# Performance work log

Measured on AMD Instinct MI355X. Metric: run time of the kernel, lower is better.

Reference implementation:

```python
import jax, jax.numpy as jnp
import numpy as np


def _kernel_features(data, proj, is_query):
    # data: [B,S,H,D], proj: [R,D] -> features [B,S,H,R]  (FAVOR+ positive softmax kernel)
    d = data.shape[-1]
    r = proj.shape[0]
    data_normalizer = 1.0 / jnp.sqrt(jnp.sqrt(jnp.float32(d)))
    ratio = 1.0 / jnp.sqrt(jnp.float32(r))
    data_hat = jnp.einsum('bshd,rd->bshr', data_normalizer * data, proj)
    diag = (jnp.sum(data * data, axis=-1) * 0.5) * (data_normalizer * data_normalizer)
    diag = diag[..., None]  # [B,S,H,1]
    if is_query:
        m = jnp.max(data_hat, axis=-1, keepdims=True)
    else:
        m = jnp.max(data_hat)
    return ratio * (jnp.exp(data_hat - diag - m) + 1e-4)


def reference(query, key, value, Wq, bq, Wk, bk, Wv, bv, Wo, bo, proj):
    proj = jax.lax.stop_gradient(proj)
    # QKV projections: [B,S,Dm] -> [B,S,H,Dh]
    q = jnp.einsum('bsd,dhk->bshk', query, Wq) + bq
    k = jnp.einsum('bsd,dhk->bshk', key, Wk) + bk
    v = jnp.einsum('bsd,dhv->bshv', value, Wv) + bv
    q_hat = _kernel_features(q, proj, True)   # [B,S,H,R]
    k_hat = _kernel_features(k, proj, False)  # [B,S,H,R]
    # kv aggregation: 'aecr,aecd->acrd'
    kv = jnp.einsum('bshr,bshv->bhrv', k_hat, v)          # [B,H,R,Dv]
    out = jnp.einsum('bshr,bhrv->bshv', q_hat, kv)        # [B,S,H,Dv]
    # normalization: k1 = sum_s k_hat ('abcd,abc->acd'), denom = q_hat . k1
    k1 = jnp.sum(k_hat, axis=1)                           # [B,H,R]
    denom = jnp.einsum('bshr,bhr->bsh', q_hat, k1)        # [B,S,H]
    out = out / denom[..., None]
    # output projection: combine heads
    return jnp.einsum('bshv,hvd->bsd', out, Wo) + bo


def setup_inputs() -> dict:
    key0 = jax.random.key(0)
    ks = jax.random.split(key0, 10)
    B, S, Dm, H, Dh, R = 4, 4096, 1024, 16, 64, 256
    scale = 1.0 / np.sqrt(Dm)
    # Gaussian orthogonal random matrix [R, Dh], scaling=0 (chi row norms)
    blk = jax.random.normal(ks[8], (R, Dh))
    qmat, _ = jnp.linalg.qr(blk)  # R >= Dh -> q is [R, Dh]
    mult = jnp.linalg.norm(jax.random.normal(ks[9], (R, Dh)), axis=1)
    proj = mult[:, None] * qmat
    return {
        'query': jax.random.normal(ks[0], (B, S, Dm)),
        'key': jax.random.normal(ks[1], (B, S, Dm)),
        'value': jax.random.normal(ks[2], (B, S, Dm)),
        'Wq': jax.random.normal(ks[3], (Dm, H, Dh)) * scale,
        'bq': jnp.zeros((H, Dh)),
        'Wk': jax.random.normal(ks[4], (Dm, H, Dh)) * scale,
        'bk': jnp.zeros((H, Dh)),
        'Wv': jax.random.normal(ks[5], (Dm, H, Dh)) * scale,
        'bv': jnp.zeros((H, Dh)),
        'Wo': jax.random.normal(ks[6], (H, Dh, Dm)) * scale,
        'bo': jnp.zeros((Dm,)),
        'proj': proj,
    }
```

## Files before the change

### kernel.cpp

```cpp
#include <hip/hip_runtime.h>

typedef unsigned short u16;
typedef unsigned int u32;
typedef __attribute__((ext_vector_type(4))) float f32x4;
typedef __attribute__((ext_vector_type(8))) short bf16x8;

#define B_ 4
#define S_ 4096
#define H_ 16
#define DH_ 64
#define R_ 256
#define DM_ 1024
#define M_ 16384
#define ROWSTR 1024

__device__ __forceinline__ float bf2f(u16 u) {
  union { u32 i; float f; } v; v.i = ((u32)u) << 16; return v.f;
}
__device__ __forceinline__ u16 f2bf(float f) {
  union { float f; u32 i; } v; v.f = f;
  u32 x = v.i;
  return (u16)((x + 0x7FFFu + ((x >> 16) & 1u)) >> 16);
}
__device__ __forceinline__ void lds_load16(const void* g, void* l) {
  __builtin_amdgcn_global_load_lds((__attribute__((address_space(1))) void*)(g),
                                   (__attribute__((address_space(3))) void*)(l), 16, 0, 0);
}
__device__ __forceinline__ int vt_idx(int dv, int s) {
  return dv * 64 + (s ^ (dv & 0x38));
}

__global__ __launch_bounds__(256) void dtype_probe_k(const u16* __restrict__ q,
                                                     int* __restrict__ flag) {
  __shared__ int cnt_s;
  int tid = threadIdx.x;
  if (tid == 0) cnt_s = 0;
  __syncthreads();
  int c = 0;
  for (int i = tid; i < 1024; i += 256) {
    u32 e = ((u32)q[i] >> 7) & 0xFF;
    c += (e >= 134) ? 1 : 0;
  }
  atomicAdd(&cnt_s, c);
  __syncthreads();
  if (tid == 0) flag[0] = (cnt_s > 32) ? 1 : 0;
}

template <int WLO>
__global__ __launch_bounds__(256) void split_k(const void* __restrict__ src,
                                               u16* __restrict__ hi, u16* __restrict__ lo,
                                               const int* __restrict__ flag) {
  const bool f32m = flag[0] != 0;
  size_t i = ((size_t)blockIdx.x * 256 + threadIdx.x) * 8;
  if (f32m) {
    f32x4 a = *(const f32x4*)((const float*)src + i);
    f32x4 b = *(const f32x4*)((const float*)src + i + 4);
    bf16x8 h, l;
    for (int e = 0; e < 4; ++e) {
      u16 ha = f2bf(a[e]); h[e] = (short)ha; l[e] = (short)f2bf(a[e] - bf2f(ha));
      u16 hb = f2bf(b[e]); h[4 + e] = (short)hb; l[4 + e] = (short)f2bf(b[e] - bf2f(hb));
    }
    *(bf16x8*)(hi + i) = h;
    if (WLO) *(bf16x8*)(lo + i) = l;
  } else {
    bf16x8 h = *(const bf16x8*)((const u16*)src + i);
    *(bf16x8*)(hi + i) = h;
    if (WLO) {
      bf16x8 z = {0, 0, 0, 0, 0, 0, 0, 0};
      *(bf16x8*)(lo + i) = z;
    }
  }
}

__global__ __launch_bounds__(256) void transpose4_k(
    const void* __restrict__ s0, const void* __restrict__ s1,
    const void* __restrict__ s2, const void* __restrict__ s3,
    u16* __restrict__ dh0, u16* __restrict__ dl0, u16* __restrict__ dh1, u16* __restrict__ dl1,
    u16* __restrict__ dh2, u16* __restrict__ dl2, u16* __restrict__ dh3, u16* __restrict__ dl3,
    const int* __restrict__ flag) {
  __shared__ float tile[32][33];
  const bool f32m = flag[0] != 0;
  int z = blockIdx.z;
  const void* src = (z == 0) ? s0 : (z == 1) ? s1 : (z == 2) ? s2 : s3;
  u16* dh = (z == 0) ? dh0 : (z == 1) ? dh1 : (z == 2) ? dh2 : dh3;
  u16* dl = (z == 0) ? dl0 : (z == 1) ? dl1 : (z == 2) ? dl2 : dl3;
  int tx = threadIdx.x, ty = threadIdx.y;
  int x0 = blockIdx.x * 32, y0 = blockIdx.y * 32;
  for (int i = ty; i < 32; i += 8) {
    size_t idx = (size_t)(y0 + i) * DM_ + x0 + tx;
    tile[i][tx] = f32m ? ((const float*)src)[idx] : bf2f(((const u16*)src)[idx]);
  }
  __syncthreads();
  for (int i = ty; i < 32; i += 8) {
    float t = tile[tx][i];
    u16 hi = f2bf(t);
    size_t o = (size_t)(x0 + i) * DM_ + y0 + tx;
    dh[o] = hi;
    dl[o] = f2bf(t - bf2f(hi));
  }
}

__global__ __launch_bounds__(256) void projcvt_k(const void* __restrict__ p,
                                                 u16* __restrict__ ph, u16* __restrict__ pl,
                                                 const int* __restrict__ flag) {
  const bool f32m = flag[0] != 0;
  int i = blockIdx.x * 256 + threadIdx.x;
  if (i < R_ * DH_) {
    float t = f32m ? ((const float*)p)[i] : bf2f(((const u16*)p)[i]);
    u16 hi = f2bf(t);
    ph[i] = hi;
    pl[i] = f2bf(t - bf2f(hi));
  }
}

template <int PREC, int OUTMODE>
__global__ __launch_bounds__(256) void gemm_k(
    const u16* __restrict__ Ah, const u16* __restrict__ Al,
    const u16* __restrict__ Bth, const u16* __restrict__ Btl,
    const void* __restrict__ bias, void* __restrict__ C, u16* __restrict__ Clo,
    const int* __restrict__ flag) {
  constexpr int NPL = (PREC == 3) ? 4 : 2;
  __shared__ __attribute__((aligned(16))) u16 pool[2 * NPL * 4096];
  const bool f32m = flag[0] != 0;
  const int K = DM_, N = DM_;
  const int tid = threadIdx.x, wave = tid >> 6, lane = tid & 63;
  const int lr = lane & 15, qd = lane >> 4;
  const int bm = blockIdx.x, bn = blockIdx.y;
  const int m0 = (wave & 1) * 64, n0 = (wave >> 1) * 64;
  const u16* Abh = Ah + (size_t)bm * 128 * K;
  const u16* Bbh = Bth + (size_t)bn * 128 * K;
  const u16* Abl = (PREC == 3) ? Al + (size_t)bm * 128 * K : nullptr;
  const u16* Bbl = (PREC == 3) ? Btl + (size_t)bn * 128 * K : nullptr;
  f32x4 zero = {0.f, 0.f, 0.f, 0.f};
  f32x4 acc[4][4];
  for (int i = 0; i < 4; ++i) for (int j = 0; j < 4; ++j) acc[i][j] = zero;

#define GEMM_STAGE(bf, kk)                                             \
  do {                                                                 \
    u16* Ph_ = pool + (bf) * (NPL * 4096);                             \
    for (int t_ = 0; t_ < 2; ++t_) {                                   \
      int c_ = wave + t_ * 4;                                          \
      int row_ = c_ * 16 + (lane >> 2);                                \
      int kc_ = (lane & 3) * 8;                                        \
      size_t go_ = (size_t)row_ * K + (kk) + kc_;                      \
      lds_load16(Abh + go_, (void*)&Ph_[c_ * 512]);                    \
      lds_load16(Bbh + go_, (void*)&Ph_[4096 + c_ * 512]);             \
      if (PREC == 3) {                                                 \
        lds_load16(Abl + go_, (void*)&Ph_[2 * 4096 + c_ * 512]);       \
        lds_load16(Bbl + go_, (void*)&Ph_[3 * 4096 + c_ * 512]);       \
      }                                                                \
    }                                                                  \
  } while (0)

  GEMM_STAGE(0, 0);
  int cur = 0;
  for (int k0 = 0; k0 < K; k0 += 32) {
    __syncthreads();
    if (k0 + 32 < K) GEMM_STAGE(cur ^ 1, k0 + 32);
    const u16* Ph = pool + cur * (NPL * 4096);
    const u16* Ash = Ph;
    const u16* Bsh = Ph + 4096;
    bf16x8 ah[4], bh[4];
    for (int i = 0; i < 4; ++i) ah[i] = *(const bf16x8*)&Ash[(m0 + i * 16 + lr) * 32 + qd * 8];
    for (int j = 0; j < 4; ++j) bh[j] = *(const bf16x8*)&Bsh[(n0 + j * 16 + lr) * 32 + qd * 8];
    for (int i = 0; i < 4; ++i)
      for (int j = 0; j < 4; ++j)
        acc[i][j] = __builtin_amdgcn_mfma_f32_16x16x32_bf16(ah[i], bh[j], acc[i][j], 0, 0, 0);
    if (PREC == 3) {
      const u16* Asl = Ph + 2 * 4096;
      const u16* Bsl = Ph + 3 * 4096;
      bf16x8 al[4], bl[4];
      for (int i = 0; i < 4; ++i) al[i] = *(const bf16x8*)&Asl[(m0 + i * 16 + lr) * 32 + qd * 8];
      for (int j = 0; j < 4; ++j) bl[j] = *(const bf16x8*)&Bsl[(n0 + j * 16 + lr) * 32 + qd * 8];
      for (int i = 0; i < 4; ++i)
        for (int j = 0; j < 4; ++j) {
          acc[i][j] = __builtin_amdgcn_mfma_f32_16x16x32_bf16(ah[i], bl[j], acc[i][j], 0, 0, 0);
          acc[i][j] = __builtin_amdgcn_mfma_f32_16x16x32_bf16(al[i], bh[j], acc[i][j], 0, 0, 0);
        }
    }
    cur ^= 1;
  }
#undef GEMM_STAGE
  for (int j = 0; j < 4; ++j) {
    int n = bn * 128 + n0 + j * 16 + lr;
    float bv = f32m ? ((const float*)bias)[n] : bf2f(((const u16*)bias)[n]);
    for (int i = 0; i < 4; ++i) {
      int mr = bm * 128 + m0 + i * 16 + qd * 4;
      for (int r2 = 0; r2 < 4; ++r2) {
        float x = acc[i][j][r2] + bv;
        size_t o = (size_t)(mr + r2) * N + n;
        if (OUTMODE == 0) {
          ((u16*)C)[o] = f2bf(x);
        } else if (OUTMODE == 1) {
          u16 hi = f2bf(x);
          ((u16*)C)[o] = hi;
          Clo[o] = f2bf(x - bf2f(hi));
        } else {
          if (f32m) ((float*)C)[o] = x;
          else ((u16*)C)[o] = f2bf(x);
        }
      }
    }
  }
}

__global__ __launch_bounds__(256) void feat_max_k(
    const u16* __restrict__ khi, const u16* __restrict__ klo,
    const u16* __restrict__ ph, const u16* __restrict__ pl, float* __restrict__ pm) {
  __shared__ __attribute__((aligned(16))) u16 kth[64 * 64];
  __shared__ __attribute__((aligned(16))) u16 ktl[64 * 64];
  __shared__ float red[4];
  const int tid = threadIdx.x, wave = tid >> 6, lane = tid & 63;
  const int lr = lane & 15, qd = lane >> 4;
  int bid = blockIdx.x;
  int chunk = bid & 63, bh = bid >> 6;
  int b = bh >> 4, h = bh & 15;
  size_t base = (((size_t)b * S_ + (size_t)chunk * 64) * H_ + h) * DH_;
  for (int t = 0; t < 2; ++t) {
    int cc = wave + t * 4;
    int rr = cc * 8 + (lane >> 3);
    int csw = (((lane & 7) ^ (rr & 7)) << 3);
    size_t go = base + (size_t)rr * ROWSTR + csw;
    lds_load16(khi + go, (void*)&kth[cc * 512]);
    lds_load16(klo + go, (void*)&ktl[cc * 512]);
  }
  __syncthreads();
  const int r0 = wave * 64;
  f32x4 zero = {0.f, 0.f, 0.f, 0.f};
  f32x4 acc[4][4];
  for (int i = 0; i < 4; ++i) for (int j = 0; j < 4; ++j) acc[i][j] = zero;
  __builtin_amdgcn_s_setprio(1);
  for (int ks = 0; ks < 2; ++ks) {
    bf16x8 ah[4], al[4], bh_[4], bl_[4];
    for (int i = 0; i < 4; ++i) {
      int cof = (ks * 32 + qd * 8) ^ ((lr & 7) << 3);
      ah[i] = *(const bf16x8*)&kth[(i * 16 + lr) * 64 + cof];
      al[i] = *(const bf16x8*)&ktl[(i * 16 + lr) * 64 + cof];
    }
    for (int j = 0; j < 4; ++j) {
      size_t o = (size_t)(r0 + j * 16 + lr) * DH_ + ks * 32 + qd * 8;
      bh_[j] = *(const bf16x8*)(ph + o);
      bl_[j] = *(const bf16x8*)(pl + o);
    }
    for (int i = 0; i < 4; ++i)
      for (int j = 0; j < 4; ++j) {
        acc[i][j] = __builtin_amdgcn_mfma_f32_16x16x32_bf16(ah[i], bh_[j], acc[i][j], 0, 0, 0);
        acc[i][j] = __builtin_amdgcn_mfma_f32_16x16x32_bf16(al[i], bh_[j], acc[i][j], 0, 0, 0);
        acc[i][j] = __builtin_amdgcn_mfma_f32_16x16x32_bf16(ah[i], bl_[j], acc[i][j], 0, 0, 0);
      }
  }
  __builtin_amdgcn_s_setprio(0);
  float mx = -3.0e38f;
  for (int i = 0; i < 4; ++i) for (int j = 0; j < 4; ++j) for (int r2 = 0; r2 < 4; ++r2)
    mx = fmaxf(mx, acc[i][j][r2]);
  for (int m2 = 1; m2 < 64; m2 <<= 1) mx = fmaxf(mx, __shfl_xor(mx, m2, 64));
  if (lane == 0) red[wave] = mx;
  __syncthreads();
  if (tid == 0)
    pm[bid] = 0.3535533905932738f * fmaxf(fmaxf(red[0], red[1]), fmaxf(red[2], red[3]));
}

__global__ __launch_bounds__(256) void reduce_max_k(const float* __restrict__ pm,
                                                    float* __restrict__ mout) {
  __shared__ float buf[256];
  int t = threadIdx.x;
  float m = -3.0e38f;
  for (int i = t; i < 4096; i += 256) m = fmaxf(m, pm[i]);
  buf[t] = m;
  __syncthreads();
  if (t < 64) {
    float v = fmaxf(fmaxf(buf[t], buf[t + 64]), fmaxf(buf[t + 128], buf[t + 192]));
    for (int m2 = 1; m2 < 64; m2 <<= 1) v = fmaxf(v, __shfl_xor(v, m2, 64));
    if (t == 0) mout[0] = v;
  }
}

__global__ __launch_bounds__(256) void kv_accum_k(
    const u16* __restrict__ khi, const u16* __restrict__ klo,
    const u16* __restrict__ vv,
    const u16* __restrict__ ph, const u16* __restrict__ pl,
    const float* __restrict__ mptr,
    float* __restrict__ pkv, float* __restrict__ pk1, int ipb) {
  __shared__ __attribute__((aligned(16))) u16 pool[256 * 72];
  __shared__ __attribute__((aligned(16))) u16 vTh[64 * 64];
  __shared__ float dpart[4][64];
  __shared__ float diagl[64];
  u16* kth = pool;
  u16* ktl = pool + 4096;
  u16* khatT = pool;
  const int tid = threadIdx.x, wave = tid >> 6, lane = tid & 63;
  const int lr = lane & 15, qd = lane >> 4;
  int bid = blockIdx.x;
  int bh = bid & 63, c = bid >> 6;
  int b = bh >> 4, h = bh & 15;
  const float mglob = mptr[0];
  const float nrm = 0.3535533905932738f;
  const float ratio = 0.0625f;
  size_t base0 = (((size_t)b * S_ + (size_t)c * ipb * 64) * H_ + h) * DH_;
  f32x4 zero = {0.f, 0.f, 0.f, 0.f};
  f32x4 acc[4][4];
  for (int i = 0; i < 4; ++i) for (int j = 0; j < 4; ++j) acc[i][j] = zero;
  float k1p[4][4];
  for (int i = 0; i < 4; ++i) for (int r2 = 0; r2 < 4; ++r2) k1p[i][r2] = 0.f;
  const int r0 = wave * 64;
  bf16x8 pfa_h[2][4], pfa_l[2][4];
  for (int ks = 0; ks < 2; ++ks)
    for (int i = 0; i < 4; ++i) {
      size_t o = (size_t)(r0 + i * 16 + lr) * DH_ + ks * 32 + qd * 8;
      pfa_h[ks][i] = *(const bf16x8*)(ph + o);
      pfa_l[ks][i] = *(const bf16x8*)(pl + o);
    }
  for (int it = 0; it < ipb; ++it) {
    size_t ibase = base0 + (size_t)it * 64 * ROWSTR;
    __syncthreads();
    for (int t = 0; t < 2; ++t) {
      int cc = wave + t * 4;
      int rr = cc * 8 + (lane >> 3);
      int csw = (((lane & 7) ^ (rr & 7)) << 3);
      size_t go = ibase + (size_t)rr * ROWSTR + csw;
      lds_load16(khi + go, (void*)&kth[cc * 512]);
      lds_load16(klo + go, (void*)&ktl[cc * 512]);
    }
    {
      int s = tid >> 2;
      int dv0 = (tid & 3) * 16;
      size_t go = ibase + (size_t)s * ROWSTR + dv0;
      bf16x8 h0 = *(const bf16x8*)(vv + go);
      bf16x8 h1 = *(const bf16x8*)(vv + go + 8);
      for (int e = 0; e < 8; ++e) {
        vTh[vt_idx(dv0 + e, s)] = (u16)h0[e];
        vTh[vt_idx(dv0 + 8 + e, s)] = (u16)h1[e];
      }
    }
    __syncthreads();
    {
      int s = tid & 63, qr = tid >> 6;
      int swz = (s & 7) << 3;
      bf16x8 h0 = *(const bf16x8*)&kth[s * 64 + ((qr * 16) ^ swz)];
      bf16x8 h1 = *(const bf16x8*)&kth[s * 64 + ((qr * 16 + 8) ^ swz)];
      bf16x8 l0 = *(const bf16x8*)&ktl[s * 64 + ((qr * 16) ^ swz)];
      bf16x8 l1 = *(const bf16x8*)&ktl[s * 64 + ((qr * 16 + 8) ^ swz)];
      float sum = 0.f;
      for (int e = 0; e < 8; ++e) { float f = bf2f((u16)h0[e]) + bf2f((u16)l0[e]); sum += f * f; }
      for (int e = 0; e < 8; ++e) { float f = bf2f((u16)h1[e]) + bf2f((u16)l1[e]); sum += f * f; }
      dpart[qr][s] = sum;
    }
    __syncthreads();
    if (tid < 64)
      diagl[tid] = 0.0625f * (dpart[0][tid] + dpart[1][tid] + dpart[2][tid] + dpart[3][tid]);
    f32x4 a1[4][4];
    for (int i = 0; i < 4; ++i) for (int j = 0; j < 4; ++j) a1[i][j] = zero;
    __builtin_amdgcn_s_setprio(1);
    for (int ks = 0; ks < 2; ++ks) {
      bf16x8 bh_[4], bl_[4];
      for (int j = 0; j < 4; ++j) {
        int cof = (ks * 32 + qd * 8) ^ ((lr & 7) << 3);
        bh_[j] = *(const bf16x8*)&kth[(j * 16 + lr) * 64 + cof];
        bl_[j] = *(const bf16x8*)&ktl[(j * 16 + lr) * 64 + cof];
      }
      for (int i = 0; i < 4; ++i)
        for (int j = 0; j < 4; ++j) {
          a1[i][j] = __builtin_amdgcn_mfma_f32_16x16x32_bf16(pfa_h[ks][i], bh_[j], a1[i][j], 0, 0, 0);
          a1[i][j] = __builtin_amdgcn_mfma_f32_16x16x32_bf16(pfa_l[ks][i], bh_[j], a1[i][j], 0, 0, 0);
          a1[i][j] = __builtin_amdgcn_mfma_f32_16x16x32_bf16(pfa_h[ks][i], bl_[j], a1[i][j], 0, 0, 0);
        }
    }
    __builtin_amdgcn_s_setprio(0);
    __syncthreads();
    for (int i = 0; i < 4; ++i)
      for (int r2 = 0; r2 < 4; ++r2) {
        int r = r0 + i * 16 + qd * 4 + r2;
        for (int j = 0; j < 4; ++j) {
          int s = j * 16 + lr;
          float arg = fminf(nrm * a1[i][j][r2] - diagl[s] - mglob, 30.f);
          float kh = ratio * (__expf(arg) + 1e-4f);
          u16 khb = f2bf(kh);
          khatT[r * 72 + s] = khb;
          k1p[i][r2] += bf2f(khb);
        }
      }
    __syncthreads();
    __builtin_amdgcn_s_setprio(1);
    for (int ks = 0; ks < 2; ++ks) {
      bf16x8 af[4], bh_[4];
      for (int i = 0; i < 4; ++i)
        af[i] = *(const bf16x8*)&khatT[(r0 + i * 16 + lr) * 72 + ks * 32 + qd * 8];
      for (int j = 0; j < 4; ++j) {
        int dv = j * 16 + lr;
        bh_[j] = *(const bf16x8*)&vTh[vt_idx(dv, ks * 32 + qd * 8)];
      }
      for (int i = 0; i < 4; ++i)
        for (int j = 0; j < 4; ++j)
          acc[i][j] = __builtin_amdgcn_mfma_f32_16x16x32_bf16(af[i], bh_[j], acc[i][j], 0, 0, 0);
    }
    __builtin_amdgcn_s_setprio(0);
  }
  size_t obase = ((size_t)c * 64 + bh) * R_;
  for (int i = 0; i < 4; ++i)
    for (int j = 0; j < 4; ++j)
      for (int r2 = 0; r2 < 4; ++r2) {
        int r = r0 + i * 16 + qd * 4 + r2;
        int dv = j * 16 + lr;
        pkv[(obase + r) * DH_ + dv] = acc[i][j][r2];
      }
  for (int i = 0; i < 4; ++i)
    for (int r2 = 0; r2 < 4; ++r2) {
      float v = k1p[i][r2];
      v += __shfl_xor(v, 1, 64); v += __shfl_xor(v, 2, 64);
      v += __shfl_xor(v, 4, 64); v += __shfl_xor(v, 8, 64);
      if (lr == 0) pk1[obase + r0 + i * 16 + qd * 4 + r2] = v;
    }
}

__global__ __launch_bounds__(256) void kv_reduce_k(
    const float* __restrict__ pkv, const float* __restrict__ pk1,
    u16* __restrict__ kvTh, u16* __restrict__ kvTl, float* __restrict__ k1, int nchunk) {
  __shared__ float tile[64][65];
  int bh = blockIdx.x, tl = blockIdx.y, t = threadIdx.x;
  if (tl == 0) {
    float s = 0.f;
    for (int c = 0; c < nchunk; ++c) s += pk1[((size_t)c * 64 + bh) * R_ + t];
    k1[(size_t)bh * R_ + t] = s;
  }
  for (int e = 0; e < 16; ++e) {
    int idx = e * 256 + t;
    int rl = idx >> 6, dv = idx & 63;
    float s = 0.f;
    for (int c = 0; c < nchunk; ++c)
      s += pkv[(((size_t)c * 64 + bh) * R_ + tl * 64 + rl) * DH_ + dv];
    tile[rl][dv] = s;
  }
  __syncthreads();
  for (int e = 0; e < 16; ++e) {
    int idx = e * 256 + t;
    int dv = idx >> 6, rl = idx & 63;
    float s = tile[rl][dv];
    u16 hi = f2bf(s);
    size_t o = ((size_t)bh * DH_ + dv) * R_ + tl * 64 + rl;
    kvTh[o] = hi;
    kvTl[o] = f2bf(s - bf2f(hi));
  }
}

__global__ __launch_bounds__(256, 4) void q_out_k(
    const u16* __restrict__ qhi, const u16* __restrict__ qlo,
    const u16* __restrict__ ph, const u16* __restrict__ pl,
    const u16* __restrict__ kvTh, const u16* __restrict__ kvTl,
    const float* __restrict__ k1, u16* __restrict__ op) {
  __shared__ __attribute__((aligned(16))) u16 pool[64 * 264];
  __shared__ float wrm[4][64];
  __shared__ float dpart[4][64];
  __shared__ float diagl[64];
  __shared__ float dinv[64];
  u16* qth = pool;
  u16* qtl = pool + 4096;
  u16* qh = pool;
  const int tid = threadIdx.x, wave = tid >> 6, lane = tid & 63;
  const int lr = lane & 15, qd = lane >> 4;
  int bid = blockIdx.x;
  int chunk = bid & 63, bh = bid >> 6;
  int b = bh >> 4, h = bh & 15;
  const float nrm = 0.3535533905932738f;
  const float ratio = 0.0625f;
  size_t base = (((size_t)b * S_ + (size_t)chunk * 64) * H_ + h) * DH_;
  const u16* kvThb = kvTh + (size_t)bh * DH_ * R_;
  const u16* kvTlb = kvTl + (size_t)bh * DH_ * R_;
  const float* k1b = k1 + (size_t)bh * R_;
  for (int t = 0; t < 2; ++t) {
    int cc = wave + t * 4;
    int rr = cc * 8 + (lane >> 3);
    int csw = (((lane & 7) ^ (rr & 7)) << 3);
    size_t go = base + (size_t)rr * ROWSTR + csw;
    lds_load16(qhi + go, (void*)&qth[cc * 512]);
    lds_load16(qlo + go, (void*)&qtl[cc * 512]);
  }
  __syncthreads();
  {
    int s = tid & 63, qr = tid >> 6;
    int swz = (s & 7) << 3;
    bf16x8 h0 = *(const bf16x8*)&qth[s * 64 + ((qr * 16) ^ swz)];
    bf16x8 h1 = *(const bf16x8*)&qth[s * 64 + ((qr * 16 + 8) ^ swz)];
    bf16x8 l0 = *(const bf16x8*)&qtl[s * 64 + ((qr * 16) ^ swz)];
    bf16x8 l1 = *(const bf16x8*)&qtl[s * 64 + ((qr * 16 + 8) ^ swz)];
    float sum = 0.f;
    for (int e = 0; e < 8; ++e) { float f = bf2f((u16)h0[e]) + bf2f((u16)l0[e]); sum += f * f; }
    for (int e = 0; e < 8; ++e) { float f = bf2f((u16)h1[e]) + bf2f((u16)l1[e]); sum += f * f; }
    dpart[qr][s] = sum;
  }
  __syncthreads();
  if (tid < 64)
    diagl[tid] = 0.0625f * (dpart[0][tid] + dpart[1][tid] + dpart[2][tid] + dpart[3][tid]);
  f32x4 zero = {0.f, 0.f, 0.f, 0.f};
  f32x4 a1[4][4];
  for (int i = 0; i < 4; ++i) for (int j = 0; j < 4; ++j) a1[i][j] = zero;
  const int r0 = wave * 64;
  __builtin_amdgcn_s_setprio(1);
  for (int ks = 0; ks < 2; ++ks) {
    bf16x8 ah[4], al[4], bh_[4], bl_[4];
    for (int i = 0; i < 4; ++i) {
      int cof = (ks * 32 + qd * 8) ^ ((lr & 7) << 3);
      ah[i] = *(const bf16x8*)&qth[(i * 16 + lr) * 64 + cof];
      al[i] = *(const bf16x8*)&qtl[(i * 16 + lr) * 64 + cof];
    }
    for (int j = 0; j < 4; ++j) {
      size_t o = (size_t)(r0 + j * 16 + lr) * DH_ + ks * 32 + qd * 8;
      bh_[j] = *(const bf16x8*)(ph + o);
      bl_[j] = *(const bf16x8*)(pl + o);
    }
    for (int i = 0; i < 4; ++i)
      for (int j = 0; j < 4; ++j) {
        a1[i][j] = __builtin_amdgcn_mfma_f32_16x16x32_bf16(ah[i], bh_[j], a1[i][j], 0, 0, 0);
        a1[i][j] = __builtin_amdgcn_mfma_f32_16x16x32_bf16(al[i], bh_[j], a1[i][j], 0, 0, 0);
        a1[i][j] = __builtin_amdgcn_mfma_f32_16x16x32_bf16(ah[i], bl_[j], a1[i][j], 0, 0, 0);
      }
  }
  __builtin_amdgcn_s_setprio(0);
  for (int i = 0; i < 4; ++i)
    for (int r2 = 0; r2 < 4; ++r2) {
      float v = fmaxf(fmaxf(a1[i][0][r2], a1[i][1][r2]), fmaxf(a1[i][2][r2], a1[i][3][r2]));
      v = fmaxf(v, __shfl_xor(v, 1, 64)); v = fmaxf(v, __shfl_xor(v, 2, 64));
      v = fmaxf(v, __shfl_xor(v, 4, 64)); v = fmaxf(v, __shfl_xor(v, 8, 64));
      if (lr == 0) wrm[wave][i * 16 + qd * 4 + r2] = v;
    }
  __syncthreads();
  float k1v[4];
  for (int j = 0; j < 4; ++j) k1v[j] = k1b[r0 + j * 16 + lr];
  for (int i = 0; i < 4; ++i)
    for (int r2 = 0; r2 < 4; ++r2) {
      int s = i * 16 + qd * 4 + r2;
      float rmax = fmaxf(fmaxf(wrm[0][s], wrm[1][s]), fmaxf(wrm[2][s], wrm[3][s]));
      float dg = diagl[s];
      float dsum = 0.f;
      for (int j = 0; j < 4; ++j) {
        float arg = fminf(nrm * (a1[i][j][r2] - rmax) - dg, 30.f);
        float qv = ratio * (__expf(arg) + 1e-4f);
        u16 qvb = f2bf(qv);
        qh[s * 264 + r0 + j * 16 + lr] = qvb;
        dsum += bf2f(qvb) * k1v[j];
      }
      dsum += __shfl_xor(dsum, 1, 64);
      dsum += __shfl_xor(dsum, 2, 64);
      dsum += __shfl_xor(dsum, 4, 64);
      dsum += __shfl_xor(dsum, 8, 64);
      if (lr == 0) dpart[wave][s] = dsum;
    }
  __syncthreads();
  if (tid < 64) {
    float dn = dpart[0][tid] + dpart[1][tid] + dpart[2][tid] + dpart[3][tid];
    dinv[tid] = 1.0f / fmaxf(dn, 1e-35f);
  }
  __syncthreads();
  f32x4 a2[2][2];
  for (int i = 0; i < 2; ++i) for (int j = 0; j < 2; ++j) a2[i][j] = zero;
  const int sw2 = (wave & 1) * 32, dw = (wave >> 1) * 32;
  __builtin_amdgcn_s_setprio(1);
  for (int ks = 0; ks < 8; ++ks) {
    bf16x8 af[2], bh_[2], bl_[2];
    for (int i = 0; i < 2; ++i)
      af[i] = *(const bf16x8*)&qh[(sw2 + i * 16 + lr) * 264 + ks * 32 + qd * 8];
    for (int j = 0; j < 2; ++j) {
      size_t o = (size_t)(dw + j * 16 + lr) * R_ + ks * 32 + qd * 8;
      bh_[j] = *(const bf16x8*)(kvThb + o);
      bl_[j] = *(const bf16x8*)(kvTlb + o);
    }
    for (int i = 0; i < 2; ++i)
      for (int j = 0; j < 2; ++j) {
        a2[i][j] = __builtin_amdgcn_mfma_f32_16x16x32_bf16(af[i], bh_[j], a2[i][j], 0, 0, 0);
        a2[i][j] = __builtin_amdgcn_mfma_f32_16x16x32_bf16(af[i], bl_[j], a2[i][j], 0, 0, 0);
      }
  }
  __builtin_amdgcn_s_setprio(0);
  for (int i = 0; i < 2; ++i)
    for (int r2 = 0; r2 < 4; ++r2) {
      int s = sw2 + i * 16 + qd * 4 + r2;
      float di = dinv[s];
      for (int j = 0; j < 2; ++j) {
        int dv = dw + j * 16 + lr;
        op[base + (size_t)s * ROWSTR + dv] = f2bf(a2[i][j][r2] * di);
      }
    }
}

extern "C" void kernel_launch(void* const* d_in, const int* in_sizes, int n_in,
                              void* d_out, int out_size, void* d_ws, size_t ws_size,
                              hipStream_t stream) {
  const void* query = d_in[0];
  const void* key   = d_in[1];
  const void* value = d_in[2];
  const void* Wq = d_in[3];
  const void* bq = d_in[4];
  const void* Wk = d_in[5];
  const void* bk = d_in[6];
  const void* Wv = d_in[7];
  const void* bv = d_in[8];
  const void* Wo = d_in[9];
  const void* bo = d_in[10];
  const void* proj = d_in[11];

  char* w = (char*)d_ws;
  const size_t MB = 1024 * 1024;
  u16* WqT_h = (u16*)(w + 0 * MB);
  u16* WqT_l = (u16*)(w + 2 * MB);
  u16* WkT_h = (u16*)(w + 4 * MB);
  u16* WkT_l = (u16*)(w + 6 * MB);
  u16* WvT_h = (u16*)(w + 8 * MB);
  u16* WvT_l = (u16*)(w + 10 * MB);
  u16* WoT_h = (u16*)(w + 12 * MB);
  u16* WoT_l = (u16*)(w + 14 * MB);
  u16* kq_hi = (u16*)(w + 16 * MB);
  u16* kq_lo = (u16*)(w + 48 * MB);
  u16* vop   = (u16*)(w + 80 * MB);
  float* pk1 = (float*)(w + 112 * MB);
  u16* kvTh  = (u16*)(w + 112 * MB + 512 * 1024);
  u16* kvTl  = (u16*)(w + 114 * MB + 512 * 1024);
  float* k1  = (float*)(w + 116 * MB + 512 * 1024);
  float* pm  = (float*)(w + 116 * MB + 640 * 1024);
  float* mg  = (float*)(w + 116 * MB + 700 * 1024);
  u16* p_hi  = (u16*)(w + 116 * MB + 768 * 1024);
  u16* p_lo  = (u16*)(w + 116 * MB + 832 * 1024);
  int* flag  = (int*)(w + 116 * MB + 900 * 1024);
  float* pkv  = (float*)(w + 117 * MB);
  u16* inA_hi = (u16*)(w + 117 * MB);
  u16* inA_lo = (u16*)(w + 149 * MB);
  int nchunk = 8;
  int ipb = 64 / nchunk;

  dtype_probe_k<<<1, 256, 0, stream>>>((const u16*)query, flag);
  transpose4_k<<<dim3(32, 32, 4), dim3(32, 8), 0, stream>>>(
      Wq, Wk, Wv, Wo, WqT_h, WqT_l, WkT_h, WkT_l, WvT_h, WvT_l, WoT_h, WoT_l, flag);
  projcvt_k<<<64, 256, 0, stream>>>(proj, p_hi, p_lo, flag);
  split_k<1><<<8192, 256, 0, stream>>>(key, inA_hi, inA_lo, flag);
  gemm_k<3, 1><<<dim3(128, 8), 256, 0, stream>>>(inA_hi, inA_lo, WkT_h, WkT_l, bk, kq_hi, kq_lo, flag);
  split_k<0><<<8192, 256, 0, stream>>>(value, inA_hi, nullptr, flag);
  gemm_k<1, 0><<<dim3(128, 8), 256, 0, stream>>>(inA_hi, nullptr, WvT_h, nullptr, bv, vop, nullptr, flag);
  feat_max_k<<<4096, 256, 0, stream>>>(kq_hi, kq_lo, p_hi, p_lo, pm);
  reduce_max_k<<<1, 256, 0, stream>>>(pm, mg);
  kv_accum_k<<<nchunk * 64, 256, 0, stream>>>(kq_hi, kq_lo, vop, p_hi, p_lo, mg, pkv, pk1, ipb);
  kv_reduce_k<<<dim3(64, 4), 256, 0, stream>>>(pkv, pk1, kvTh, kvTl, k1, nchunk);
  split_k<1><<<8192, 256, 0, stream>>>(query, inA_hi, inA_lo, flag);
  gemm_k<3, 1><<<dim3(128, 8), 256, 0, stream>>>(inA_hi, inA_lo, WqT_h, WqT_l, bq, kq_hi, kq_lo, flag);
  q_out_k<<<4096, 256, 0, stream>>>(kq_hi, kq_lo, p_hi, p_lo, kvTh, kvTl, k1, vop);
  gemm_k<1, 2><<<dim3(128, 8), 256, 0, stream>>>(vop, nullptr, WoT_h, nullptr, bo, d_out, nullptr, flag);
}
```

Measured before the change: 849.6 us.

## Fuse global key max into kv accumulation with online rescaling; compute diag in GEMM epilogue

Removes the separate feat_max_k pass, which recomputed the key feature projection only to find the global max. kv_accum_k now keeps a running per-chunk max and rescales its partial kv and k1 sums flash-style. kv_reduce_k reweights the chunks by exp(chunk_max - global_max) and adds the 1e-4 term analytically using per-chunk value sums. The squared-norm diag is now computed in the Q/K GEMM epilogue instead of being recomputed in both feature kernels, and the chunk count doubles to 16. The trade-off is extra rescaling work and shuffles, the removal of the exp-argument clamp, and slightly different rounding.

```diff
diff --git a/kernel.cpp b/kernel.cpp
--- a/kernel.cpp
+++ b/kernel.cpp
@@ -118,7 +118,7 @@
     const u16* __restrict__ Ah, const u16* __restrict__ Al,
     const u16* __restrict__ Bth, const u16* __restrict__ Btl,
     const void* __restrict__ bias, void* __restrict__ C, u16* __restrict__ Clo,
-    const int* __restrict__ flag) {
+    float* __restrict__ diag, const int* __restrict__ flag) {
   constexpr int NPL = (PREC == 3) ? 4 : 2;
   __shared__ __attribute__((aligned(16))) u16 pool[2 * NPL * 4096];
   const bool f32m = flag[0] != 0;
@@ -181,6 +181,9 @@
     cur ^= 1;
   }
 #undef GEMM_STAGE
+  float dq[16];
+  if (OUTMODE == 1)
+    for (int t = 0; t < 16; ++t) dq[t] = 0.f;
   for (int j = 0; j < 4; ++j) {
     int n = bn * 128 + n0 + j * 16 + lr;
     float bv = f32m ? ((const float*)bias)[n] : bf2f(((const u16*)bias)[n]);
@@ -192,6 +195,7 @@
         if (OUTMODE == 0) {
           ((u16*)C)[o] = f2bf(x);
         } else if (OUTMODE == 1) {
+          dq[i * 4 + r2] += x * x;
           u16 hi = f2bf(x);
           ((u16*)C)[o] = hi;
           Clo[o] = f2bf(x - bf2f(hi));
@@ -202,70 +206,26 @@
       }
     }
   }
-}
-
-__global__ __launch_bounds__(256) void feat_max_k(
-    const u16* __restrict__ khi, const u16* __restrict__ klo,
-    const u16* __restrict__ ph, const u16* __restrict__ pl, float* __restrict__ pm) {
-  __shared__ __attribute__((aligned(16))) u16 kth[64 * 64];
-  __shared__ __attribute__((aligned(16))) u16 ktl[64 * 64];
-  __shared__ float red[4];
-  const int tid = threadIdx.x, wave = tid >> 6, lane = tid & 63;
-  const int lr = lane & 15, qd = lane >> 4;
-  int bid = blockIdx.x;
-  int chunk = bid & 63, bh = bid >> 6;
-  int b = bh >> 4, h = bh & 15;
-  size_t base = (((size_t)b * S_ + (size_t)chunk * 64) * H_ + h) * DH_;
-  for (int t = 0; t < 2; ++t) {
-    int cc = wave + t * 4;
-    int rr = cc * 8 + (lane >> 3);
-    int csw = (((lane & 7) ^ (rr & 7)) << 3);
-    size_t go = base + (size_t)rr * ROWSTR + csw;
-    lds_load16(khi + go, (void*)&kth[cc * 512]);
-    lds_load16(klo + go, (void*)&ktl[cc * 512]);
-  }
-  __syncthreads();
-  const int r0 = wave * 64;
-  f32x4 zero = {0.f, 0.f, 0.f, 0.f};
-  f32x4 acc[4][4];
-  for (int i = 0; i < 4; ++i) for (int j = 0; j < 4; ++j) acc[i][j] = zero;
-  __builtin_amdgcn_s_setprio(1);
-  for (int ks = 0; ks < 2; ++ks) {
-    bf16x8 ah[4], al[4], bh_[4], bl_[4];
-    for (int i = 0; i < 4; ++i) {
-      int cof = (ks * 32 + qd * 8) ^ ((lr & 7) << 3);
-      ah[i] = *(const bf16x8*)&kth[(i * 16 + lr) * 64 + cof];
-      al[i] = *(const bf16x8*)&ktl[(i * 16 + lr) * 64 + cof];
-    }
-    for (int j = 0; j < 4; ++j) {
-      size_t o = (size_t)(r0 + j * 16 + lr) * DH_ + ks * 32 + qd * 8;
-      bh_[j] = *(const bf16x8*)(ph + o);
-      bl_[j] = *(const bf16x8*)(pl + o);
-    }
-    for (int i = 0; i < 4; ++i)
-      for (int j = 0; j < 4; ++j) {
-        acc[i][j] = __builtin_amdgcn_mfma_f32_16x16x32_bf16(ah[i], bh_[j], acc[i][j], 0, 0, 0);
-        acc[i][j] = __builtin_amdgcn_mfma_f32_16x16x32_bf16(al[i], bh_[j], acc[i][j], 0, 0, 0);
-        acc[i][j] = __builtin_amdgcn_mfma_f32_16x16x32_bf16(ah[i], bl_[j], acc[i][j], 0, 0, 0);
-      }
-  }
-  __builtin_amdgcn_s_setprio(0);
-  float mx = -3.0e38f;
-  for (int i = 0; i < 4; ++i) for (int j = 0; j < 4; ++j) for (int r2 = 0; r2 < 4; ++r2)
-    mx = fmaxf(mx, acc[i][j][r2]);
-  for (int m2 = 1; m2 < 64; m2 <<= 1) mx = fmaxf(mx, __shfl_xor(mx, m2, 64));
-  if (lane == 0) red[wave] = mx;
-  __syncthreads();
-  if (tid == 0)
-    pm[bid] = 0.3535533905932738f * fmaxf(fmaxf(red[0], red[1]), fmaxf(red[2], red[3]));
+  if (OUTMODE == 1) {
+    int h = (bn * 128 + n0) >> 6;
+    for (int t = 0; t < 16; ++t) {
+      float v = dq[t];
+      v += __shfl_xor(v, 1, 64); v += __shfl_xor(v, 2, 64);
+      v += __shfl_xor(v, 4, 64); v += __shfl_xor(v, 8, 64);
+      if (lr == 0) {
+        int mrow = bm * 128 + m0 + (t >> 2) * 16 + qd * 4 + (t & 3);
+        diag[(size_t)mrow * H_ + h] = 0.0625f * v;
+      }
+    }
+  }
 }
 
 __global__ __launch_bounds__(256) void reduce_max_k(const float* __restrict__ pm,
-                                                    float* __restrict__ mout) {
+                                                    float* __restrict__ mout, int n) {
   __shared__ float buf[256];
   int t = threadIdx.x;
   float m = -3.0e38f;
-  for (int i = t; i < 4096; i += 256) m = fmaxf(m, pm[i]);
+  for (int i = t; i < n; i += 256) m = fmaxf(m, pm[i]);
   buf[t] = m;
   __syncthreads();
   if (t < 64) {
@@ -279,12 +239,13 @@
     const u16* __restrict__ khi, const u16* __restrict__ klo,
     const u16* __restrict__ vv,
     const u16* __restrict__ ph, const u16* __restrict__ pl,
-    const float* __restrict__ mptr,
-    float* __restrict__ pkv, float* __restrict__ pk1, int ipb) {
+    const float* __restrict__ diagk,
+    float* __restrict__ pkv, float* __restrict__ pk1,
+    float* __restrict__ pvs, float* __restrict__ pmc, int ipb) {
   __shared__ __attribute__((aligned(16))) u16 pool[256 * 72];
   __shared__ __attribute__((aligned(16))) u16 vTh[64 * 64];
-  __shared__ float dpart[4][64];
   __shared__ float diagl[64];
+  __shared__ float red[4];
   u16* kth = pool;
   u16* ktl = pool + 4096;
   u16* khatT = pool;
@@ -293,15 +254,17 @@
   int bid = blockIdx.x;
   int bh = bid & 63, c = bid >> 6;
   int b = bh >> 4, h = bh & 15;
-  const float mglob = mptr[0];
   const float nrm = 0.3535533905932738f;
-  const float ratio = 0.0625f;
   size_t base0 = (((size_t)b * S_ + (size_t)c * ipb * 64) * H_ + h) * DH_;
+  int grow0 = b * S_ + c * ipb * 64;
   f32x4 zero = {0.f, 0.f, 0.f, 0.f};
   f32x4 acc[4][4];
   for (int i = 0; i < 4; ++i) for (int j = 0; j < 4; ++j) acc[i][j] = zero;
   float k1p[4][4];
   for (int i = 0; i < 4; ++i) for (int r2 = 0; r2 < 4; ++r2) k1p[i][r2] = 0.f;
+  float mr = -3.0e38f;
+  float vs[16];
+  for (int e = 0; e < 16; ++e) vs[e] = 0.f;
   const int r0 = wave * 64;
   bf16x8 pfa_h[2][4], pfa_l[2][4];
   for (int ks = 0; ks < 2; ++ks)
@@ -321,6 +284,7 @@
       lds_load16(khi + go, (void*)&kth[cc * 512]);
       lds_load16(klo + go, (void*)&ktl[cc * 512]);
     }
+    if (tid < 64) diagl[tid] = diagk[(size_t)(grow0 + it * 64 + tid) * H_ + h];
     {
       int s = tid >> 2;
       int dv0 = (tid & 3) * 16;
@@ -330,24 +294,11 @@
       for (int e = 0; e < 8; ++e) {
         vTh[vt_idx(dv0 + e, s)] = (u16)h0[e];
         vTh[vt_idx(dv0 + 8 + e, s)] = (u16)h1[e];
+        vs[e] += bf2f((u16)h0[e]);
+        vs[8 + e] += bf2f((u16)h1[e]);
       }
     }
     __syncthreads();
-    {
-      int s = tid & 63, qr = tid >> 6;
-      int swz = (s & 7) << 3;
-      bf16x8 h0 = *(const bf16x8*)&kth[s * 64 + ((qr * 16) ^ swz)];
-      bf16x8 h1 = *(const bf16x8*)&kth[s * 64 + ((qr * 16 + 8) ^ swz)];
-      bf16x8 l0 = *(const bf16x8*)&ktl[s * 64 + ((qr * 16) ^ swz)];
-      bf16x8 l1 = *(const bf16x8*)&ktl[s * 64 + ((qr * 16 + 8) ^ swz)];
-      float sum = 0.f;
-      for (int e = 0; e < 8; ++e) { float f = bf2f((u16)h0[e]) + bf2f((u16)l0[e]); sum += f * f; }
-      for (int e = 0; e < 8; ++e) { float f = bf2f((u16)h1[e]) + bf2f((u16)l1[e]); sum += f * f; }
-      dpart[qr][s] = sum;
-    }
-    __syncthreads();
-    if (tid < 64)
-      diagl[tid] = 0.0625f * (dpart[0][tid] + dpart[1][tid] + dpart[2][tid] + dpart[3][tid]);
     f32x4 a1[4][4];
     for (int i = 0; i < 4; ++i) for (int j = 0; j < 4; ++j) a1[i][j] = zero;
     __builtin_amdgcn_s_setprio(1);
@@ -366,15 +317,27 @@
         }
     }
     __builtin_amdgcn_s_setprio(0);
+    float mx = -3.0e38f;
+    for (int i = 0; i < 4; ++i) for (int j = 0; j < 4; ++j) for (int r2 = 0; r2 < 4; ++r2)
+      mx = fmaxf(mx, a1[i][j][r2]);
+    for (int m2 = 1; m2 < 64; m2 <<= 1) mx = fmaxf(mx, __shfl_xor(mx, m2, 64));
+    if (lane == 0) red[wave] = mx;
     __syncthreads();
+    float cm = nrm * fmaxf(fmaxf(red[0], red[1]), fmaxf(red[2], red[3]));
+    if (cm > mr) {
+      float sc = __expf(mr - cm);
+      for (int i = 0; i < 4; ++i) for (int j = 0; j < 4; ++j)
+        for (int r2 = 0; r2 < 4; ++r2) acc[i][j][r2] *= sc;
+      for (int i = 0; i < 4; ++i) for (int r2 = 0; r2 < 4; ++r2) k1p[i][r2] *= sc;
+      mr = cm;
+    }
     for (int i = 0; i < 4; ++i)
       for (int r2 = 0; r2 < 4; ++r2) {
         int r = r0 + i * 16 + qd * 4 + r2;
         for (int j = 0; j < 4; ++j) {
           int s = j * 16 + lr;
-          float arg = fminf(nrm * a1[i][j][r2] - diagl[s] - mglob, 30.f);
-          float kh = ratio * (__expf(arg) + 1e-4f);
-          u16 khb = f2bf(kh);
+          float arg = nrm * a1[i][j][r2] - diagl[s] - mr;
+          u16 khb = f2bf(__expf(arg));
           khatT[r * 72 + s] = khb;
           k1p[i][r2] += bf2f(khb);
         }
@@ -410,25 +373,53 @@
       v += __shfl_xor(v, 4, 64); v += __shfl_xor(v, 8, 64);
       if (lr == 0) pk1[obase + r0 + i * 16 + qd * 4 + r2] = v;
     }
+  if (tid == 0) pmc[bid] = mr;
+  __syncthreads();
+  float* fbuf = (float*)pool;
+  {
+    int srow = tid >> 2, g = tid & 3;
+    for (int e = 0; e < 16; ++e) fbuf[srow * 64 + g * 16 + e] = vs[e];
+  }
+  __syncthreads();
+  if (tid < 64) {
+    float s = 0.f;
+    for (int r = 0; r < 64; ++r) s += fbuf[r * 64 + tid];
+    pvs[(size_t)bid * 64 + tid] = s;
+  }
 }
 
 __global__ __launch_bounds__(256) void kv_reduce_k(
     const float* __restrict__ pkv, const float* __restrict__ pk1,
+    const float* __restrict__ pvs, const float* __restrict__ pmc,
+    const float* __restrict__ mg,
     u16* __restrict__ kvTh, u16* __restrict__ kvTl, float* __restrict__ k1, int nchunk) {
   __shared__ float tile[64][65];
+  __shared__ float wbuf[16];
+  __shared__ float vbuf[64];
   int bh = blockIdx.x, tl = blockIdx.y, t = threadIdx.x;
+  const float ratio = 0.0625f;
+  float mg0 = mg[0];
+  if (t < nchunk) wbuf[t] = __expf(pmc[(size_t)t * 64 + bh] - mg0);
+  if (t >= 64 && t < 128) {
+    int dv = t - 64;
+    float s = 0.f;
+    for (int c2 = 0; c2 < nchunk; ++c2) s += pvs[((size_t)c2 * 64 + bh) * 64 + dv];
+    vbuf[dv] = s;
+  }
+  __syncthreads();
   if (tl == 0) {
     float s = 0.f;
-    for (int c = 0; c < nchunk; ++c) s += pk1[((size_t)c * 64 + bh) * R_ + t];
-    k1[(size_t)bh * R_ + t] = s;
+    for (int c2 = 0; c2 < nchunk; ++c2)
+      s += wbuf[c2] * pk1[((size_t)c2 * 64 + bh) * R_ + t];
+    k1[(size_t)bh * R_ + t] = ratio * (s + 1e-4f * (float)S_);
   }
   for (int e = 0; e < 16; ++e) {
     int idx = e * 256 + t;
     int rl = idx >> 6, dv = idx & 63;
     float s = 0.f;
-    for (int c = 0; c < nchunk; ++c)
-      s += pkv[(((size_t)c * 64 + bh) * R_ + tl * 64 + rl) * DH_ + dv];
-    tile[rl][dv] = s;
+    for (int c2 = 0; c2 < nchunk; ++c2)
+      s += wbuf[c2] * pkv[(((size_t)c2 * 64 + bh) * R_ + tl * 64 + rl) * DH_ + dv];
+    tile[rl][dv] = ratio * (s + 1e-4f * vbuf[dv]);
   }
   __syncthreads();
   for (int e = 0; e < 16; ++e) {
@@ -446,7 +437,8 @@
     const u16* __restrict__ qhi, const u16* __restrict__ qlo,
     const u16* __restrict__ ph, const u16* __restrict__ pl,
     const u16* __restrict__ kvTh, const u16* __restrict__ kvTl,
-    const float* __restrict__ k1, u16* __restrict__ op) {
+    const float* __restrict__ k1, const float* __restrict__ diagq,
+    u16* __restrict__ op) {
   __shared__ __attribute__((aligned(16))) u16 pool[64 * 264];
   __shared__ float wrm[4][64];
   __shared__ float dpart[4][64];
@@ -474,22 +466,8 @@
     lds_load16(qhi + go, (void*)&qth[cc * 512]);
     lds_load16(qlo + go, (void*)&qtl[cc * 512]);
   }
-  __syncthreads();
-  {
-    int s = tid & 63, qr = tid >> 6;
-    int swz = (s & 7) << 3;
-    bf16x8 h0 = *(const bf16x8*)&qth[s * 64 + ((qr * 16) ^ swz)];
-    bf16x8 h1 = *(const bf16x8*)&qth[s * 64 + ((qr * 16 + 8) ^ swz)];
-    bf16x8 l0 = *(const bf16x8*)&qtl[s * 64 + ((qr * 16) ^ swz)];
-    bf16x8 l1 = *(const bf16x8*)&qtl[s * 64 + ((qr * 16 + 8) ^ swz)];
-    float sum = 0.f;
-    for (int e = 0; e < 8; ++e) { float f = bf2f((u16)h0[e]) + bf2f((u16)l0[e]); sum += f * f; }
-    for (int e = 0; e < 8; ++e) { float f = bf2f((u16)h1[e]) + bf2f((u16)l1[e]); sum += f * f; }
-    dpart[qr][s] = sum;
-  }
-  __syncthreads();
-  if (tid < 64)
-    diagl[tid] = 0.0625f * (dpart[0][tid] + dpart[1][tid] + dpart[2][tid] + dpart[3][tid]);
+  if (tid < 64) diagl[tid] = diagq[(size_t)(b * S_ + chunk * 64 + tid) * H_ + h];
+  __syncthreads();
   f32x4 zero = {0.f, 0.f, 0.f, 0.f};
   f32x4 a1[4][4];
   for (int i = 0; i < 4; ++i) for (int j = 0; j < 4; ++j) a1[i][j] = zero;
@@ -532,7 +510,7 @@
       float dg = diagl[s];
       float dsum = 0.f;
       for (int j = 0; j < 4; ++j) {
-        float arg = fminf(nrm * (a1[i][j][r2] - rmax) - dg, 30.f);
+        float arg = nrm * (a1[i][j][r2] - rmax) - dg;
         float qv = ratio * (__expf(arg) + 1e-4f);
         u16 qvb = f2bf(qv);
         qh[s * 264 + r0 + j * 16 + lr] = qvb;
@@ -610,11 +588,11 @@
   u16* kq_hi = (u16*)(w + 16 * MB);
   u16* kq_lo = (u16*)(w + 48 * MB);
   u16* vop   = (u16*)(w + 80 * MB);
-  float* pk1 = (float*)(w + 112 * MB);
+  float* pvs = (float*)(w + 112 * MB);
   u16* kvTh  = (u16*)(w + 112 * MB + 512 * 1024);
   u16* kvTl  = (u16*)(w + 114 * MB + 512 * 1024);
   float* k1  = (float*)(w + 116 * MB + 512 * 1024);
-  float* pm  = (float*)(w + 116 * MB + 640 * 1024);
+  float* pmc = (float*)(w + 116 * MB + 640 * 1024);
   float* mg  = (float*)(w + 116 * MB + 700 * 1024);
   u16* p_hi  = (u16*)(w + 116 * MB + 768 * 1024);
   u16* p_lo  = (u16*)(w + 116 * MB + 832 * 1024);
@@ -622,7 +600,9 @@
   float* pkv  = (float*)(w + 117 * MB);
   u16* inA_hi = (u16*)(w + 117 * MB);
   u16* inA_lo = (u16*)(w + 149 * MB);
-  int nchunk = 8;
+  float* diag_b = (float*)(w + 181 * MB);
+  float* pk1b   = (float*)(w + 182 * MB);
+  int nchunk = 16;
   int ipb = 64 / nchunk;
 
   dtype_probe_k<<<1, 256, 0, stream>>>((const u16*)query, flag);
@@ -630,15 +610,14 @@
       Wq, Wk, Wv, Wo, WqT_h, WqT_l, WkT_h, WkT_l, WvT_h, WvT_l, WoT_h, WoT_l, flag);
   projcvt_k<<<64, 256, 0, stream>>>(proj, p_hi, p_lo, flag);
   split_k<1><<<8192, 256, 0, stream>>>(key, inA_hi, inA_lo, flag);
-  gemm_k<3, 1><<<dim3(128, 8), 256, 0, stream>>>(inA_hi, inA_lo, WkT_h, WkT_l, bk, kq_hi, kq_lo, flag);
+  gemm_k<3, 1><<<dim3(128, 8), 256, 0, stream>>>(inA_hi, inA_lo, WkT_h, WkT_l, bk, kq_hi, kq_lo, diag_b, flag);
   split_k<0><<<8192, 256, 0, stream>>>(value, inA_hi, nullptr, flag);
-  gemm_k<1, 0><<<dim3(128, 8), 256, 0, stream>>>(inA_hi, nullptr, WvT_h, nullptr, bv, vop, nullptr, flag);
-  feat_max_k<<<4096, 256, 0, stream>>>(kq_hi, kq_lo, p_hi, p_lo, pm);
-  reduce_max_k<<<1, 256, 0, stream>>>(pm, mg);
-  kv_accum_k<<<nchunk * 64, 256, 0, stream>>>(kq_hi, kq_lo, vop, p_hi, p_lo, mg, pkv, pk1, ipb);
-  kv_reduce_k<<<dim3(64, 4), 256, 0, stream>>>(pkv, pk1, kvTh, kvTl, k1, nchunk);
+  gemm_k<1, 0><<<dim3(128, 8), 256, 0, stream>>>(inA_hi, nullptr, WvT_h, nullptr, bv, vop, nullptr, nullptr, flag);
+  kv_accum_k<<<nchunk * 64, 256, 0, stream>>>(kq_hi, kq_lo, vop, p_hi, p_lo, diag_b, pkv, pk1b, pvs, pmc, ipb);
+  reduce_max_k<<<1, 256, 0, stream>>>(pmc, mg, nchunk * 64);
+  kv_reduce_k<<<dim3(64, 4), 256, 0, stream>>>(pkv, pk1b, pvs, pmc, mg, kvTh, kvTl, k1, nchunk);
   split_k<1><<<8192, 256, 0, stream>>>(query, inA_hi, inA_lo, flag);
-  gemm_k<3, 1><<<dim3(128, 8), 256, 0, stream>>>(inA_hi, inA_lo, WqT_h, WqT_l, bq, kq_hi, kq_lo, flag);
-  q_out_k<<<4096, 256, 0, stream>>>(kq_hi, kq_lo, p_hi, p_lo, kvTh, kvTl, k1, vop);
-  gemm_k<1, 2><<<dim3(128, 8), 256, 0, stream>>>(vop, nullptr, WoT_h, nullptr, bo, d_out, nullptr, flag);
-}
+  gemm_k<3, 1><<<dim3(128, 8), 256, 0, stream>>>(inA_hi, inA_lo, WqT_h, WqT_l, bq, kq_hi, kq_lo, diag_b, flag);
+  q_out_k<<<4096, 256, 0, stream>>>(kq_hi, kq_lo, p_hi, p_lo, kvTh, kvTl, k1, diag_b, vop);
+  gemm_k<1, 2><<<dim3(128, 8), 256, 0, stream>>>(vop, nullptr, WoT_h, nullptr, bo, d_out, nullptr, nullptr, flag);
+}
```

Result: no change. 863.0 us (+1.6%).
